# Performance work log

Measured on AMD Instinct MI355X. Metric: run time of the kernel, lower is better.

Reference implementation:

```python
import jax, jax.numpy as jnp
import numpy as np

N_NODES = 100000
N_EDGES = 1600000
IN_DIM = 64
HID_DIM = 64
OUT_DIM = 1


def setup_inputs() -> dict:
    key = jax.random.key(0)
    ks = jax.random.split(key, 5)
    x = jax.random.normal(ks[0], (N_NODES, IN_DIM), dtype=jnp.float32)
    edge_index = jax.random.randint(ks[1], (2, N_EDGES), 0, N_NODES, dtype=jnp.int64)
    s1 = 1.0 / np.sqrt(IN_DIM)
    s2 = 1.0 / np.sqrt(HID_DIM)
    W1 = jax.random.normal(ks[2], (IN_DIM, HID_DIM), dtype=jnp.float32) * s1
    b1 = jnp.zeros((HID_DIM,), dtype=jnp.float32)
    W2 = jax.random.normal(ks[3], (HID_DIM, HID_DIM), dtype=jnp.float32) * s2
    b2 = jnp.zeros((HID_DIM,), dtype=jnp.float32)
    Wp = jax.random.normal(ks[4], (HID_DIM, OUT_DIM), dtype=jnp.float32) * s2
    bp = jnp.zeros((OUT_DIM,), dtype=jnp.float32)
    return {"x": x, "edge_index": edge_index, "W1": W1, "b1": b1,
            "W2": W2, "b2": b2, "Wp": Wp, "bp": bp}


def _gcn_conv(x, src, dst, deg_inv_sqrt, W, b):
    # PyG GCNConv: linear transform, then deg-normalized scatter-add aggregation
    h = x @ W  # [N, out]
    norm = deg_inv_sqrt[src] * deg_inv_sqrt[dst]  # [E_total]
    msg = h[src] * norm[:, None]  # gather + scale, [E_total, out]
    agg = jax.ops.segment_sum(msg, dst, num_segments=x.shape[0])
    return agg + b


def reference(x, edge_index, W1, b1, W2, b2, Wp, bp):
    n = x.shape[0]
    # add self-loops (as PyG GCNConv does by default)
    loop = jnp.arange(n, dtype=edge_index.dtype)
    src = jnp.concatenate([edge_index[0], loop])
    dst = jnp.concatenate([edge_index[1], loop])
    # symmetric normalization from in-degree over dst (includes self-loops)
    deg = jax.ops.segment_sum(jnp.ones_like(dst, dtype=x.dtype), dst, num_segments=n)
    deg_inv_sqrt = jnp.where(deg > 0, jax.lax.rsqrt(jnp.maximum(deg, 1e-12)), 0.0)
    h = jax.nn.relu(_gcn_conv(x, src, dst, deg_inv_sqrt, W1, b1))
    # dropout(p=0.3) is identity at eval time
    h = jax.nn.relu(_gcn_conv(h, src, dst, deg_inv_sqrt, W2, b2))
    return h @ Wp + bp  # [N, OUT_DIM]
```

## Files before the change

kernel.cpp:

```cpp
#include <hip/hip_runtime.h>
#include <hip/hip_fp16.h>


#define GNN_N 100000
#define GNN_E 1600000
#define NBUCK 391
#define HBLK  500
#define EPBH  3200
#define NBLK  250
#define EPB   6400
#define SCTILE 16
#define STAGE_CAP 4864
#define DUMMY_OFF (GNN_N * 128)

typedef _Float16 half8 __attribute__((ext_vector_type(8)));
typedef float f32x4 __attribute__((ext_vector_type(4)));

__global__ __launch_bounds__(256) void k_hist(const int* __restrict__ dst,
                                              int* __restrict__ hist,
                                              __half* __restrict__ TA,
                                              __half* __restrict__ TB) {
    __shared__ int h[NBUCK];
    for (int i = threadIdx.x; i < NBUCK; i += 256) h[i] = 0;
    if (blockIdx.x == 0 && threadIdx.x < 16) {
        uint4 z = {0, 0, 0, 0};
        int t = threadIdx.x;
        __half* base = (t < 8) ? TA : TB;
        *(uint4*)((char*)base + DUMMY_OFF + (t & 7) * 16) = z;
    }
    __syncthreads();
    int b = blockIdx.x;
    int e0 = b * EPBH, e1 = min(e0 + EPBH, GNN_E);
    for (int e = e0 + threadIdx.x * 4; e < e1; e += 1024) {
        int4 d = *(const int4*)(dst + e);
        atomicAdd(&h[d.x >> 8], 1);
        atomicAdd(&h[d.y >> 8], 1);
        atomicAdd(&h[d.z >> 8], 1);
        atomicAdd(&h[d.w >> 8], 1);
    }
    __syncthreads();
    for (int i = threadIdx.x; i < NBUCK; i += 256)
        hist[b * NBUCK + i] = h[i];
}

__global__ __launch_bounds__(256) void k_cscan(int* __restrict__ hist,
                                               int* __restrict__ tot) {
    __shared__ int tile[256][SCTILE + 1];
    int k0 = blockIdx.x * SCTILE;
    int b = threadIdx.x;
    int lane = b & 63, w = b >> 6;
    int cSub = lane >> 4;
    int l16 = lane & 15;
    int col = w * 4 + cSub;
    int run = 0;
    for (int pass = 0; pass < 2; ++pass) {
        int r = pass * 256 + b;
#pragma unroll
        for (int i = 0; i < SCTILE; ++i) {
            int k = k0 + i;
            tile[b][i] = (k < NBUCK && r < HBLK) ? hist[r * NBUCK + k] : 0;
        }
        __syncthreads();
        for (int chunk = 0; chunk < 16; ++chunk) {
            int idx = chunk * 16 + l16;
            int v = tile[idx][col];
            int s = v;
#pragma unroll
            for (int o = 1; o < 16; o <<= 1) {
                int t = __shfl_up(s, o);
                if (l16 >= o) s += t;
            }
            tile[idx][col] = s - v + run;
            run += __shfl(s, lane | 15);
        }
        __syncthreads();
#pragma unroll
        for (int i = 0; i < SCTILE; ++i) {
            int k = k0 + i;
            if (k < NBUCK && r < HBLK) hist[r * NBUCK + k] = tile[b][i];
        }
        __syncthreads();
    }
    if (l16 == 0 && k0 + col < NBUCK) tot[k0 + col] = run;
}

__global__ __launch_bounds__(512) void k_btot(const int* __restrict__ tot,
                                              int* __restrict__ bbase,
                                              int* __restrict__ cbase) {
    __shared__ int s[512];
    int t = threadIdx.x;
    int own = (t < NBUCK) ? tot[t] : 0;
    s[t] = own;
    __syncthreads();
    for (int off = 1; off < 512; off <<= 1) {
        int v = (t >= off) ? s[t - off] : 0;
        __syncthreads();
        s[t] += v;
        __syncthreads();
    }
    if (t < NBUCK) {
        int ex = s[t] - own;
        bbase[t] = ex;
        cbase[t] = (ex & ~3) + t * 772;
    }
    if (t == 0) bbase[NBUCK] = GNN_E;
}

__global__ __launch_bounds__(256) void k_part(const int* __restrict__ src,
                                              const int* __restrict__ dst,
                                              const int* __restrict__ hist,
                                              const int* __restrict__ bbase,
                                              unsigned int* __restrict__ part) {
    __shared__ int off[NBUCK];
    int b = blockIdx.x;
    for (int i = threadIdx.x; i < NBUCK; i += 256)
        off[i] = bbase[i] + hist[(2 * b) * NBUCK + i];
    __syncthreads();
    int e0 = b * EPB, e1 = min(e0 + EPB, GNN_E);
    for (int e = e0 + threadIdx.x * 4; e < e1; e += 1024) {
        int4 d = *(const int4*)(dst + e);
        int4 s = *(const int4*)(src + e);
        int sl0 = atomicAdd(&off[d.x >> 8], 1);
        part[sl0] = ((unsigned int)(d.x & 255) << 17) | (unsigned int)s.x;
        int sl1 = atomicAdd(&off[d.y >> 8], 1);
        part[sl1] = ((unsigned int)(d.y & 255) << 17) | (unsigned int)s.y;
        int sl2 = atomicAdd(&off[d.z >> 8], 1);
        part[sl2] = ((unsigned int)(d.z & 255) << 17) | (unsigned int)s.z;
        int sl3 = atomicAdd(&off[d.w >> 8], 1);
        part[sl3] = ((unsigned int)(d.w & 255) << 17) | (unsigned int)s.w;
    }
}

__global__ __launch_bounds__(256) void k_bsort(const unsigned int* __restrict__ part,
                                               const int* __restrict__ bbase,
                                               const int* __restrict__ cbase,
                                               int* __restrict__ csr,
                                               int* __restrict__ rowptr,
                                               int* __restrict__ deg,
                                               float* __restrict__ dis) {
    __shared__ int cnt[256];
    __shared__ int pstart[256];
    __shared__ int bump[256];
    __shared__ int wtot[4];
    __shared__ unsigned int stage[STAGE_CAP];
    int k = blockIdx.x;
    int t = threadIdx.x;
    cnt[t] = 0;
    __syncthreads();
    int e0 = bbase[k], e1 = bbase[k + 1];
    int m = e1 - e0;
    bool fits = (m <= STAGE_CAP);
    for (int i = t; i < m; i += 256) {
        unsigned int p = part[e0 + i];
        if (fits) stage[i] = p;
        atomicAdd(&cnt[p >> 17], 1);
    }
    __syncthreads();
    int c = cnt[t];
    int padded = (c + 3) & ~3;
    int v = padded;
#pragma unroll
    for (int o = 1; o < 64; o <<= 1) {
        int u = __shfl_up(v, o);
        if ((t & 63) >= o) v += u;
    }
    if ((t & 63) == 63) wtot[t >> 6] = v;
    __syncthreads();
    int wb = 0;
#pragma unroll
    for (int j = 0; j < 4; ++j)
        if (j < (t >> 6)) wb += wtot[j];
    pstart[t] = wb + v - padded;
    bump[t] = pstart[t];
    __syncthreads();
    int cb = cbase[k];
    int node = k * 256 + t;
    if (node < GNN_N) {
        rowptr[node] = cb + pstart[t];
        deg[node]    = padded;
        dis[node]    = rsqrtf((float)c + 1.0f);
    }
    for (int i = t; i < m; i += 256) {
        unsigned int p = fits ? stage[i] : part[e0 + i];
        int slot = atomicAdd(&bump[p >> 17], 1);
        csr[cb + slot] = (int)(p & 0x1FFFF) << 7;
    }
    __syncthreads();
    if (node < GNN_N) {
        for (int i = c; i < padded; ++i)
            csr[cb + pstart[t] + i] = DUMMY_OFF;
    }
}

__global__ __launch_bounds__(256) void k_mmf(const float* __restrict__ X,
                                             const float* __restrict__ W,
                                             const float* __restrict__ dis,
                                             __half* __restrict__ Y, int n) {
    __shared__ __align__(16) __half Xs[64][72];
    __shared__ __align__(16) __half Wt[64][72];
    __shared__ float disS[64];
    int tid = threadIdx.x;
    int base = blockIdx.x * 64;
    for (int i = tid; i < 4096; i += 256) {
        int k = i >> 6, j = i & 63;
        Wt[j][k] = __float2half(W[i]);
    }
    if (tid < 64) disS[tid] = (base + tid < n) ? dis[base + tid] : 0.f;
#pragma unroll
    for (int ii = 0; ii < 4; ++ii) {
        int i = ii * 256 + tid;
        int r = i >> 4, c4 = i & 15;
        int row = base + r;
        float4 vv = (row < n) ? ((const float4*)(X + (size_t)row * 64))[c4]
                              : make_float4(0.f, 0.f, 0.f, 0.f);
        *(__half2*)&Xs[r][c4 * 4 + 0] = __floats2half2_rn(vv.x, vv.y);
        *(__half2*)&Xs[r][c4 * 4 + 2] = __floats2half2_rn(vv.z, vv.w);
    }
    __syncthreads();
    int w = tid >> 6, lane = tid & 63;
    int ar = w * 16 + (lane & 15);
    int ak = (lane >> 4) * 8;
    half8 a0 = *(const half8*)&Xs[ar][ak];
    half8 a1 = *(const half8*)&Xs[ar][32 + ak];
    f32x4 acc0 = {0.f, 0.f, 0.f, 0.f}, acc1 = acc0, acc2 = acc0, acc3 = acc0;
#define MMCOL(ACC, C) {                                                   \
        half8 b0 = *(const half8*)&Wt[(C) * 16 + (lane & 15)][ak];        \
        half8 b1 = *(const half8*)&Wt[(C) * 16 + (lane & 15)][32 + ak];   \
        ACC = __builtin_amdgcn_mfma_f32_16x16x32_f16(a0, b0, ACC, 0, 0, 0); \
        ACC = __builtin_amdgcn_mfma_f32_16x16x32_f16(a1, b1, ACC, 0, 0, 0); }
    MMCOL(acc0, 0) MMCOL(acc1, 1) MMCOL(acc2, 2) MMCOL(acc3, 3)
#undef MMCOL
    __syncthreads();
#define DST(ACC, C) {                                                     \
        _Pragma("unroll")                                                 \
        for (int i = 0; i < 4; ++i) {                                     \
            int rl = w * 16 + (lane >> 4) * 4 + i;                        \
            Xs[rl][(C) * 16 + (lane & 15)] = __float2half(ACC[i] * disS[rl]); \
        } }
    DST(acc0, 0) DST(acc1, 1) DST(acc2, 2) DST(acc3, 3)
#undef DST
    __syncthreads();
#pragma unroll
    for (int ii = 0; ii < 2; ++ii) {
        int i = ii * 256 + tid;
        int r = i >> 3, c8 = i & 7;
        int row = base + r;
        if (row < n)
            *(uint4*)(Y + (size_t)row * 64 + c8 * 8) = *(const uint4*)&Xs[r][c8 * 8];
    }
}

#define ACC8(A, U) {                                                     \
    float2 f_;                                                           \
    f_ = __half22float2(*(__half2*)&U.x); A[0] += f_.x; A[1] += f_.y;    \
    f_ = __half22float2(*(__half2*)&U.y); A[2] += f_.x; A[3] += f_.y;    \
    f_ = __half22float2(*(__half2*)&U.z); A[4] += f_.x; A[5] += f_.y;    \
    f_ = __half22float2(*(__half2*)&U.w); A[6] += f_.x; A[7] += f_.y; }

__global__ __launch_bounds__(256) void k_gatherW2(
        const __half* __restrict__ T, const int* __restrict__ csr,
        const int* __restrict__ rowptr, const int* __restrict__ deg,
        const float* __restrict__ dis, const float* __restrict__ bias,
        const float* __restrict__ W2, __half* __restrict__ TB) {
    __shared__ __align__(16) __half Wt[64][72];
    __shared__ __align__(16) __half Rt[32][72];
    __shared__ float disT[32];
    int tid = threadIdx.x;
    for (int i = tid; i < 4096; i += 256) {
        int k = i >> 6, j = i & 63;
        Wt[j][k] = __float2half(W2[i]);
    }
    int q = tid & 7;
    int nl = tid >> 3;
    int node = blockIdx.x * 32 + nl;
    int base = rowptr[node];
    int cnt  = deg[node];
    float dd = dis[node];
    if (q == 0) disT[nl] = dd;
    const char* Tq = (const char*)T + q * 16;
    float a0[8], a1[8];
#pragma unroll
    for (int i = 0; i < 8; ++i) { a0[i] = 0.f; a1[i] = 0.f; }
    int j = 0;
    for (; j + 8 <= cnt; j += 8) {
        int4 c0 = *(const int4*)(csr + base + j);
        int4 c1 = *(const int4*)(csr + base + j + 4);
        uint4 u0 = *(const uint4*)(Tq + (size_t)(unsigned)c0.x);
        uint4 u1 = *(const uint4*)(Tq + (size_t)(unsigned)c0.y);
        uint4 u2 = *(const uint4*)(Tq + (size_t)(unsigned)c0.z);
        uint4 u3 = *(const uint4*)(Tq + (size_t)(unsigned)c0.w);
        uint4 u4 = *(const uint4*)(Tq + (size_t)(unsigned)c1.x);
        uint4 u5 = *(const uint4*)(Tq + (size_t)(unsigned)c1.y);
        uint4 u6 = *(const uint4*)(Tq + (size_t)(unsigned)c1.z);
        uint4 u7 = *(const uint4*)(Tq + (size_t)(unsigned)c1.w);
        ACC8(a0, u0) ACC8(a1, u1) ACC8(a0, u2) ACC8(a1, u3)
        ACC8(a0, u4) ACC8(a1, u5) ACC8(a0, u6) ACC8(a1, u7)
    }
    if (j < cnt) {
        int4 c0 = *(const int4*)(csr + base + j);
        uint4 u0 = *(const uint4*)(Tq + (size_t)(unsigned)c0.x);
        uint4 u1 = *(const uint4*)(Tq + (size_t)(unsigned)c0.y);
        uint4 u2 = *(const uint4*)(Tq + (size_t)(unsigned)c0.z);
        uint4 u3 = *(const uint4*)(Tq + (size_t)(unsigned)c0.w);
        ACC8(a0, u0) ACC8(a1, u1) ACC8(a0, u2) ACC8(a1, u3)
    }
    uint4 us = *(const uint4*)(Tq + (size_t)node * 128);
    ACC8(a1, us)
    float4 bb0 = ((const float4*)bias)[q * 2 + 0];
    float4 bb1 = ((const float4*)bias)[q * 2 + 1];
    float r[8];
    r[0] = fmaxf(dd * (a0[0] + a1[0]) + bb0.x, 0.f);
    r[1] = fmaxf(dd * (a0[1] + a1[1]) + bb0.y, 0.f);
    r[2] = fmaxf(dd * (a0[2] + a1[2]) + bb0.z, 0.f);
    r[3] = fmaxf(dd * (a0[3] + a1[3]) + bb0.w, 0.f);
    r[4] = fmaxf(dd * (a0[4] + a1[4]) + bb1.x, 0.f);
    r[5] = fmaxf(dd * (a0[5] + a1[5]) + bb1.y, 0.f);
    r[6] = fmaxf(dd * (a0[6] + a1[6]) + bb1.z, 0.f);
    r[7] = fmaxf(dd * (a0[7] + a1[7]) + bb1.w, 0.f);
    uint4 u;
    *(__half2*)&u.x = __floats2half2_rn(r[0], r[1]);
    *(__half2*)&u.y = __floats2half2_rn(r[2], r[3]);
    *(__half2*)&u.z = __floats2half2_rn(r[4], r[5]);
    *(__half2*)&u.w = __floats2half2_rn(r[6], r[7]);
    *(uint4*)&Rt[nl][q * 8] = u;
    __syncthreads();
    int w = tid >> 6, lane = tid & 63;
    int band = w >> 1, cg = w & 1;
    int ar = band * 16 + (lane & 15);
    int ak = (lane >> 4) * 8;
    half8 fa0 = *(const half8*)&Rt[ar][ak];
    half8 fa1 = *(const half8*)&Rt[ar][32 + ak];
    f32x4 acc0 = {0.f, 0.f, 0.f, 0.f}, acc1 = acc0;
    {
        int c0 = cg * 2, c1 = cg * 2 + 1;
        half8 b00 = *(const half8*)&Wt[c0 * 16 + (lane & 15)][ak];
        half8 b01 = *(const half8*)&Wt[c0 * 16 + (lane & 15)][32 + ak];
        half8 b10 = *(const half8*)&Wt[c1 * 16 + (lane & 15)][ak];
        half8 b11 = *(const half8*)&Wt[c1 * 16 + (lane & 15)][32 + ak];
        acc0 = __builtin_amdgcn_mfma_f32_16x16x32_f16(fa0, b00, acc0, 0, 0, 0);
        acc0 = __builtin_amdgcn_mfma_f32_16x16x32_f16(fa1, b01, acc0, 0, 0, 0);
        acc1 = __builtin_amdgcn_mfma_f32_16x16x32_f16(fa0, b10, acc1, 0, 0, 0);
        acc1 = __builtin_amdgcn_mfma_f32_16x16x32_f16(fa1, b11, acc1, 0, 0, 0);
    }
    __syncthreads();
#pragma unroll
    for (int i = 0; i < 4; ++i) {
        int rl = band * 16 + (lane >> 4) * 4 + i;
        float dsc = disT[rl];
        Rt[rl][(cg * 2 + 0) * 16 + (lane & 15)] = __float2half(acc0[i] * dsc);
        Rt[rl][(cg * 2 + 1) * 16 + (lane & 15)] = __float2half(acc1[i] * dsc);
    }
    __syncthreads();
    {
        int r8 = tid >> 3, c8 = tid & 7;
        int row = blockIdx.x * 32 + r8;
        *(uint4*)(TB + (size_t)row * 64 + c8 * 8) = *(const uint4*)&Rt[r8][c8 * 8];
    }
}

__global__ __launch_bounds__(256) void k_gatherg(
        const __half* __restrict__ T, const int* __restrict__ csr,
        const int* __restrict__ rowptr, const int* __restrict__ deg,
        const float* __restrict__ dis, const float* __restrict__ bias,
        const float* __restrict__ Wp, const float* __restrict__ bp,
        float* __restrict__ out, int n) {
    int tid = threadIdx.x;
    int q = tid & 7;
    int node = blockIdx.x * 32 + (tid >> 3);
    if (node >= n) return;
    int base = rowptr[node];
    int cnt  = deg[node];
    float dd = dis[node];
    const char* Tq = (const char*)T + q * 16;
    float a0[8], a1[8];
#pragma unroll
    for (int i = 0; i < 8; ++i) { a0[i] = 0.f; a1[i] = 0.f; }
    int j = 0;
    for (; j + 8 <= cnt; j += 8) {
        int4 c0 = *(const int4*)(csr + base + j);
        int4 c1 = *(const int4*)(csr + base + j + 4);
        uint4 u0 = *(const uint4*)(Tq + (size_t)(unsigned)c0.x);
        uint4 u1 = *(const uint4*)(Tq + (size_t)(unsigned)c0.y);
        uint4 u2 = *(const uint4*)(Tq + (size_t)(unsigned)c0.z);
        uint4 u3 = *(const uint4*)(Tq + (size_t)(unsigned)c0.w);
        uint4 u4 = *(const uint4*)(Tq + (size_t)(unsigned)c1.x);
        uint4 u5 = *(const uint4*)(Tq + (size_t)(unsigned)c1.y);
        uint4 u6 = *(const uint4*)(Tq + (size_t)(unsigned)c1.z);
        uint4 u7 = *(const uint4*)(Tq + (size_t)(unsigned)c1.w);
        ACC8(a0, u0) ACC8(a1, u1) ACC8(a0, u2) ACC8(a1, u3)
        ACC8(a0, u4) ACC8(a1, u5) ACC8(a0, u6) ACC8(a1, u7)
    }
    if (j < cnt) {
        int4 c0 = *(const int4*)(csr + base + j);
        uint4 u0 = *(const uint4*)(Tq + (size_t)(unsigned)c0.x);
        uint4 u1 = *(const uint4*)(Tq + (size_t)(unsigned)c0.y);
        uint4 u2 = *(const uint4*)(Tq + (size_t)(unsigned)c0.z);
        uint4 u3 = *(const uint4*)(Tq + (size_t)(unsigned)c0.w);
        ACC8(a0, u0) ACC8(a1, u1) ACC8(a0, u2) ACC8(a1, u3)
    }
    uint4 us = *(const uint4*)(Tq + (size_t)node * 128);
    ACC8(a1, us)
    float4 bb0 = ((const float4*)bias)[q * 2 + 0];
    float4 bb1 = ((const float4*)bias)[q * 2 + 1];
    float r[8];
    r[0] = fmaxf(dd * (a0[0] + a1[0]) + bb0.x, 0.f);
    r[1] = fmaxf(dd * (a0[1] + a1[1]) + bb0.y, 0.f);
    r[2] = fmaxf(dd * (a0[2] + a1[2]) + bb0.z, 0.f);
    r[3] = fmaxf(dd * (a0[3] + a1[3]) + bb0.w, 0.f);
    r[4] = fmaxf(dd * (a0[4] + a1[4]) + bb1.x, 0.f);
    r[5] = fmaxf(dd * (a0[5] + a1[5]) + bb1.y, 0.f);
    r[6] = fmaxf(dd * (a0[6] + a1[6]) + bb1.z, 0.f);
    r[7] = fmaxf(dd * (a0[7] + a1[7]) + bb1.w, 0.f);
    float4 w0 = ((const float4*)Wp)[q * 2 + 0];
    float4 w1 = ((const float4*)Wp)[q * 2 + 1];
    float s = r[0] * w0.x + r[1] * w0.y + r[2] * w0.z + r[3] * w0.w
            + r[4] * w1.x + r[5] * w1.y + r[6] * w1.z + r[7] * w1.w;
#pragma unroll
    for (int m = 1; m <= 4; m <<= 1) s += __shfl_xor(s, m);
    if (q == 0) out[node] = s + bp[0];
}

extern "C" void kernel_launch(void* const* d_in, const int* in_sizes, int n_in,
                              void* d_out, int out_size, void* d_ws, size_t ws_size,
                              hipStream_t stream) {
    const float* x  = (const float*)d_in[0];
    const int*   ei = (const int*)d_in[1];
    const float* W1 = (const float*)d_in[2];
    const float* b1 = (const float*)d_in[3];
    const float* W2 = (const float*)d_in[4];
    const float* b2 = (const float*)d_in[5];
    const float* Wp = (const float*)d_in[6];
    const float* bp = (const float*)d_in[7];
    float* out = (float*)d_out;

    const int N = GNN_N, E = GNN_E;
    const int* srcv = ei;
    const int* dstv = ei + E;

    char* ws = (char*)d_ws;
    int*    hist   = (int*)(ws + 0);
    int*    bbase  = (int*)(ws + 784000);
    int*    cbase  = (int*)(ws + 785600);
    int*    rowptr = (int*)(ws + 787200);
    int*    deg    = (int*)(ws + 1187200);
    float*  dis    = (float*)(ws + 1587200);
    int*    tot    = (int*)(ws + 1587200);
    int*    csr    = (int*)(ws + 1987200);
    __half* TA     = (__half*)(ws + 9597440);
    __half* TB     = (__half*)(ws + 22400000);
    unsigned int* part = (unsigned int*)(ws + 35200256);

    k_hist <<<HBLK, 256, 0, stream>>>(dstv, hist, TA, TB);
    k_cscan<<<(NBUCK + SCTILE - 1) / SCTILE, 256, 0, stream>>>(hist, tot);
    k_btot <<<1, 512, 0, stream>>>(tot, bbase, cbase);
    k_part <<<NBLK, 256, 0, stream>>>(srcv, dstv, hist, bbase, part);
    k_bsort<<<NBUCK, 256, 0, stream>>>(part, bbase, cbase, csr, rowptr, deg, dis);

    k_mmf<<<(N + 63) / 64, 256, 0, stream>>>(x, W1, dis, TA, N);
    k_gatherW2<<<N / 32, 256, 0, stream>>>(TA, csr, rowptr, deg, dis, b1, W2, TB);
    k_gatherg<<<(N + 31) / 32, 256, 0, stream>>>(TB, csr, rowptr, deg, dis,
                                                 b2, Wp, bp, out, N);
}
```

Baseline: 127.5 us.

## Fuse CSR build kernels into one cooperative kernel with grid syncs

Merges the five CSR construction kernels (histogram, column scan, bucket total scan, partition, bucket sort) into a single cooperative launch separated by grid-wide barriers, with shared memory overlaid through a union. This removes four kernel launch boundaries and their gaps. The partition phase now uses 500 blocks of 3200 edges instead of 250 blocks of 6400, matching the histogram granularity. The trade-off is grid.sync cost, a larger LDS footprint (about 21 KB for the staging buffer) held by every block, and a requirement that all 500 blocks be co-resident.

Result: slower. 361.6 us (+183.5%).

```diff
diff --git a/kernel.cpp b/kernel.cpp
--- a/kernel.cpp
+++ b/kernel.cpp
@@ -1,14 +1,15 @@
 #include <hip/hip_runtime.h>
 #include <hip/hip_fp16.h>
+#include <hip/hip_cooperative_groups.h>
+
+namespace cg = cooperative_groups;
 
 
 #define GNN_N 100000
 #define GNN_E 1600000
 #define NBUCK 391
-#define HBLK  500
-#define EPBH  3200
-#define NBLK  250
-#define EPB   6400
+#define CBLK  500
+#define EPB   3200
 #define SCTILE 16
 #define STAGE_CAP 4864
 #define DUMMY_OFF (GNN_N * 128)
@@ -16,179 +17,195 @@
 typedef _Float16 half8 __attribute__((ext_vector_type(8)));
 typedef float f32x4 __attribute__((ext_vector_type(4)));
 
-__global__ __launch_bounds__(256) void k_hist(const int* __restrict__ dst,
-                                              int* __restrict__ hist,
-                                              __half* __restrict__ TA,
-                                              __half* __restrict__ TB) {
-    __shared__ int h[NBUCK];
-    for (int i = threadIdx.x; i < NBUCK; i += 256) h[i] = 0;
-    if (blockIdx.x == 0 && threadIdx.x < 16) {
+union CsrLds {
+    int h[NBUCK];
+    int tile[256][SCTILE + 1];
+    int s[512];
+    int off[NBUCK];
+    struct {
+        int cnt[256];
+        int pstart[256];
+        int bump[256];
+        int wtot[4];
+        unsigned int stage[STAGE_CAP];
+    } p5;
+};
+
+__global__ __launch_bounds__(256) void k_csr(const int* __restrict__ src,
+                                             const int* __restrict__ dst,
+                                             int* __restrict__ hist,
+                                             int* __restrict__ bbase,
+                                             int* __restrict__ cbase,
+                                             int* __restrict__ tot,
+                                             unsigned int* __restrict__ part,
+                                             int* __restrict__ csr,
+                                             int* __restrict__ rowptr,
+                                             int* __restrict__ deg,
+                                             float* __restrict__ dis,
+                                             __half* __restrict__ TA,
+                                             __half* __restrict__ TB) {
+    cg::grid_group grid = cg::this_grid();
+    __shared__ CsrLds u;
+    int bid = blockIdx.x;
+    int t = threadIdx.x;
+
+    for (int i = t; i < NBUCK; i += 256) u.h[i] = 0;
+    if (bid == 0 && t < 16) {
         uint4 z = {0, 0, 0, 0};
-        int t = threadIdx.x;
         __half* base = (t < 8) ? TA : TB;
         *(uint4*)((char*)base + DUMMY_OFF + (t & 7) * 16) = z;
     }
     __syncthreads();
-    int b = blockIdx.x;
-    int e0 = b * EPBH, e1 = min(e0 + EPBH, GNN_E);
-    for (int e = e0 + threadIdx.x * 4; e < e1; e += 1024) {
-        int4 d = *(const int4*)(dst + e);
-        atomicAdd(&h[d.x >> 8], 1);
-        atomicAdd(&h[d.y >> 8], 1);
-        atomicAdd(&h[d.z >> 8], 1);
-        atomicAdd(&h[d.w >> 8], 1);
-    }
-    __syncthreads();
-    for (int i = threadIdx.x; i < NBUCK; i += 256)
-        hist[b * NBUCK + i] = h[i];
-}
-
-__global__ __launch_bounds__(256) void k_cscan(int* __restrict__ hist,
-                                               int* __restrict__ tot) {
-    __shared__ int tile[256][SCTILE + 1];
-    int k0 = blockIdx.x * SCTILE;
-    int b = threadIdx.x;
-    int lane = b & 63, w = b >> 6;
-    int cSub = lane >> 4;
-    int l16 = lane & 15;
-    int col = w * 4 + cSub;
-    int run = 0;
-    for (int pass = 0; pass < 2; ++pass) {
-        int r = pass * 256 + b;
-#pragma unroll
-        for (int i = 0; i < SCTILE; ++i) {
-            int k = k0 + i;
-            tile[b][i] = (k < NBUCK && r < HBLK) ? hist[r * NBUCK + k] : 0;
-        }
-        __syncthreads();
-        for (int chunk = 0; chunk < 16; ++chunk) {
-            int idx = chunk * 16 + l16;
-            int v = tile[idx][col];
-            int s = v;
-#pragma unroll
-            for (int o = 1; o < 16; o <<= 1) {
-                int t = __shfl_up(s, o);
-                if (l16 >= o) s += t;
+    {
+        int e0 = bid * EPB, e1 = min(e0 + EPB, GNN_E);
+        for (int e = e0 + t * 4; e < e1; e += 1024) {
+            int4 d = *(const int4*)(dst + e);
+            atomicAdd(&u.h[d.x >> 8], 1);
+            atomicAdd(&u.h[d.y >> 8], 1);
+            atomicAdd(&u.h[d.z >> 8], 1);
+            atomicAdd(&u.h[d.w >> 8], 1);
+        }
+        __syncthreads();
+        for (int i = t; i < NBUCK; i += 256)
+            hist[bid * NBUCK + i] = u.h[i];
+    }
+    grid.sync();
+
+    if (bid < (NBUCK + SCTILE - 1) / SCTILE) {
+        int k0 = bid * SCTILE;
+        int lane = t & 63, w = t >> 6;
+        int cSub = lane >> 4;
+        int l16 = lane & 15;
+        int col = w * 4 + cSub;
+        int run = 0;
+        for (int pass = 0; pass < 2; ++pass) {
+            int r = pass * 256 + t;
+#pragma unroll
+            for (int i = 0; i < SCTILE; ++i) {
+                int k = k0 + i;
+                u.tile[t][i] = (k < NBUCK && r < CBLK) ? hist[r * NBUCK + k] : 0;
             }
-            tile[idx][col] = s - v + run;
-            run += __shfl(s, lane | 15);
-        }
-        __syncthreads();
-#pragma unroll
-        for (int i = 0; i < SCTILE; ++i) {
-            int k = k0 + i;
-            if (k < NBUCK && r < HBLK) hist[r * NBUCK + k] = tile[b][i];
-        }
-        __syncthreads();
-    }
-    if (l16 == 0 && k0 + col < NBUCK) tot[k0 + col] = run;
-}
-
-__global__ __launch_bounds__(512) void k_btot(const int* __restrict__ tot,
-                                              int* __restrict__ bbase,
-                                              int* __restrict__ cbase) {
-    __shared__ int s[512];
-    int t = threadIdx.x;
-    int own = (t < NBUCK) ? tot[t] : 0;
-    s[t] = own;
-    __syncthreads();
-    for (int off = 1; off < 512; off <<= 1) {
-        int v = (t >= off) ? s[t - off] : 0;
-        __syncthreads();
-        s[t] += v;
-        __syncthreads();
-    }
-    if (t < NBUCK) {
-        int ex = s[t] - own;
-        bbase[t] = ex;
-        cbase[t] = (ex & ~3) + t * 772;
-    }
-    if (t == 0) bbase[NBUCK] = GNN_E;
-}
-
-__global__ __launch_bounds__(256) void k_part(const int* __restrict__ src,
-                                              const int* __restrict__ dst,
-                                              const int* __restrict__ hist,
-                                              const int* __restrict__ bbase,
-                                              unsigned int* __restrict__ part) {
-    __shared__ int off[NBUCK];
-    int b = blockIdx.x;
-    for (int i = threadIdx.x; i < NBUCK; i += 256)
-        off[i] = bbase[i] + hist[(2 * b) * NBUCK + i];
-    __syncthreads();
-    int e0 = b * EPB, e1 = min(e0 + EPB, GNN_E);
-    for (int e = e0 + threadIdx.x * 4; e < e1; e += 1024) {
-        int4 d = *(const int4*)(dst + e);
-        int4 s = *(const int4*)(src + e);
-        int sl0 = atomicAdd(&off[d.x >> 8], 1);
-        part[sl0] = ((unsigned int)(d.x & 255) << 17) | (unsigned int)s.x;
-        int sl1 = atomicAdd(&off[d.y >> 8], 1);
-        part[sl1] = ((unsigned int)(d.y & 255) << 17) | (unsigned int)s.y;
-        int sl2 = atomicAdd(&off[d.z >> 8], 1);
-        part[sl2] = ((unsigned int)(d.z & 255) << 17) | (unsigned int)s.z;
-        int sl3 = atomicAdd(&off[d.w >> 8], 1);
-        part[sl3] = ((unsigned int)(d.w & 255) << 17) | (unsigned int)s.w;
-    }
-}
-
-__global__ __launch_bounds__(256) void k_bsort(const unsigned int* __restrict__ part,
-                                               const int* __restrict__ bbase,
-                                               const int* __restrict__ cbase,
-                                               int* __restrict__ csr,
-                                               int* __restrict__ rowptr,
-                                               int* __restrict__ deg,
-                                               float* __restrict__ dis) {
-    __shared__ int cnt[256];
-    __shared__ int pstart[256];
-    __shared__ int bump[256];
-    __shared__ int wtot[4];
-    __shared__ unsigned int stage[STAGE_CAP];
-    int k = blockIdx.x;
-    int t = threadIdx.x;
-    cnt[t] = 0;
-    __syncthreads();
-    int e0 = bbase[k], e1 = bbase[k + 1];
-    int m = e1 - e0;
-    bool fits = (m <= STAGE_CAP);
-    for (int i = t; i < m; i += 256) {
-        unsigned int p = part[e0 + i];
-        if (fits) stage[i] = p;
-        atomicAdd(&cnt[p >> 17], 1);
-    }
-    __syncthreads();
-    int c = cnt[t];
-    int padded = (c + 3) & ~3;
-    int v = padded;
-#pragma unroll
-    for (int o = 1; o < 64; o <<= 1) {
-        int u = __shfl_up(v, o);
-        if ((t & 63) >= o) v += u;
-    }
-    if ((t & 63) == 63) wtot[t >> 6] = v;
-    __syncthreads();
-    int wb = 0;
-#pragma unroll
-    for (int j = 0; j < 4; ++j)
-        if (j < (t >> 6)) wb += wtot[j];
-    pstart[t] = wb + v - padded;
-    bump[t] = pstart[t];
-    __syncthreads();
-    int cb = cbase[k];
-    int node = k * 256 + t;
-    if (node < GNN_N) {
-        rowptr[node] = cb + pstart[t];
-        deg[node]    = padded;
-        dis[node]    = rsqrtf((float)c + 1.0f);
-    }
-    for (int i = t; i < m; i += 256) {
-        unsigned int p = fits ? stage[i] : part[e0 + i];
-        int slot = atomicAdd(&bump[p >> 17], 1);
-        csr[cb + slot] = (int)(p & 0x1FFFF) << 7;
-    }
-    __syncthreads();
-    if (node < GNN_N) {
-        for (int i = c; i < padded; ++i)
-            csr[cb + pstart[t] + i] = DUMMY_OFF;
+            __syncthreads();
+            for (int chunk = 0; chunk < 16; ++chunk) {
+                int idx = chunk * 16 + l16;
+                int v = u.tile[idx][col];
+                int s = v;
+#pragma unroll
+                for (int o = 1; o < 16; o <<= 1) {
+                    int tt = __shfl_up(s, o);
+                    if (l16 >= o) s += tt;
+                }
+                u.tile[idx][col] = s - v + run;
+                run += __shfl(s, lane | 15);
+            }
+            __syncthreads();
+#pragma unroll
+            for (int i = 0; i < SCTILE; ++i) {
+                int k = k0 + i;
+                if (k < NBUCK && r < CBLK) hist[r * NBUCK + k] = u.tile[t][i];
+            }
+            __syncthreads();
+        }
+        if (l16 == 0 && k0 + col < NBUCK) tot[k0 + col] = run;
+    }
+    grid.sync();
+
+    if (bid == 0) {
+        int own0 = (t < NBUCK) ? tot[t] : 0;
+        int own1 = (t + 256 < NBUCK) ? tot[t + 256] : 0;
+        u.s[t] = own0;
+        u.s[t + 256] = own1;
+        __syncthreads();
+        for (int off = 1; off < 512; off <<= 1) {
+            int a = (t >= off) ? u.s[t - off] : 0;
+            int b = (t + 256 >= off) ? u.s[t + 256 - off] : 0;
+            __syncthreads();
+            u.s[t] += a;
+            u.s[t + 256] += b;
+            __syncthreads();
+        }
+        if (t < NBUCK) {
+            int ex = u.s[t] - own0;
+            bbase[t] = ex;
+            cbase[t] = (ex & ~3) + t * 772;
+        }
+        if (t + 256 < NBUCK) {
+            int ex = u.s[t + 256] - own1;
+            bbase[t + 256] = ex;
+            cbase[t + 256] = (ex & ~3) + (t + 256) * 772;
+        }
+        if (t == 0) bbase[NBUCK] = GNN_E;
+    }
+    grid.sync();
+
+    for (int i = t; i < NBUCK; i += 256)
+        u.off[i] = bbase[i] + hist[bid * NBUCK + i];
+    __syncthreads();
+    {
+        int e0 = bid * EPB, e1 = min(e0 + EPB, GNN_E);
+        for (int e = e0 + t * 4; e < e1; e += 1024) {
+            int4 d = *(const int4*)(dst + e);
+            int4 s = *(const int4*)(src + e);
+            int sl0 = atomicAdd(&u.off[d.x >> 8], 1);
+            part[sl0] = ((unsigned int)(d.x & 255) << 17) | (unsigned int)s.x;
+            int sl1 = atomicAdd(&u.off[d.y >> 8], 1);
+            part[sl1] = ((unsigned int)(d.y & 255) << 17) | (unsigned int)s.y;
+            int sl2 = atomicAdd(&u.off[d.z >> 8], 1);
+            part[sl2] = ((unsigned int)(d.z & 255) << 17) | (unsigned int)s.z;
+            int sl3 = atomicAdd(&u.off[d.w >> 8], 1);
+            part[sl3] = ((unsigned int)(d.w & 255) << 17) | (unsigned int)s.w;
+        }
+    }
+    grid.sync();
+
+    if (bid < NBUCK) {
+        int k = bid;
+        u.p5.cnt[t] = 0;
+        __syncthreads();
+        int e0 = bbase[k], e1 = bbase[k + 1];
+        int m = e1 - e0;
+        bool fits = (m <= STAGE_CAP);
+        for (int i = t; i < m; i += 256) {
+            unsigned int p = part[e0 + i];
+            if (fits) u.p5.stage[i] = p;
+            atomicAdd(&u.p5.cnt[p >> 17], 1);
+        }
+        __syncthreads();
+        int c = u.p5.cnt[t];
+        int padded = (c + 3) & ~3;
+        int v = padded;
+#pragma unroll
+        for (int o = 1; o < 64; o <<= 1) {
+            int uu = __shfl_up(v, o);
+            if ((t & 63) >= o) v += uu;
+        }
+        if ((t & 63) == 63) u.p5.wtot[t >> 6] = v;
+        __syncthreads();
+        int wb = 0;
+#pragma unroll
+        for (int j = 0; j < 4; ++j)
+            if (j < (t >> 6)) wb += u.p5.wtot[j];
+        int ps = wb + v - padded;
+        u.p5.pstart[t] = ps;
+        u.p5.bump[t] = ps;
+        __syncthreads();
+        int cb = cbase[k];
+        int node = k * 256 + t;
+        if (node < GNN_N) {
+            rowptr[node] = cb + ps;
+            deg[node]    = padded;
+            dis[node]    = rsqrtf((float)c + 1.0f);
+        }
+        for (int i = t; i < m; i += 256) {
+            unsigned int p = fits ? u.p5.stage[i] : part[e0 + i];
+            int slot = atomicAdd(&u.p5.bump[p >> 17], 1);
+            csr[cb + slot] = (int)(p & 0x1FFFF) << 7;
+        }
+        __syncthreads();
+        if (node < GNN_N) {
+            for (int i = c; i < padded; ++i)
+                csr[cb + ps + i] = DUMMY_OFF;
+        }
     }
 }
 
@@ -325,14 +342,14 @@
     *(uint4*)&Rt[nl][q * 8] = u;
     __syncthreads();
     int w = tid >> 6, lane = tid & 63;
-    int band = w >> 1, cg = w & 1;
+    int band = w >> 1, cg2 = w & 1;
     int ar = band * 16 + (lane & 15);
     int ak = (lane >> 4) * 8;
     half8 fa0 = *(const half8*)&Rt[ar][ak];
     half8 fa1 = *(const half8*)&Rt[ar][32 + ak];
     f32x4 acc0 = {0.f, 0.f, 0.f, 0.f}, acc1 = acc0;
     {
-        int c0 = cg * 2, c1 = cg * 2 + 1;
+        int c0 = cg2 * 2, c1 = cg2 * 2 + 1;
         half8 b00 = *(const half8*)&Wt[c0 * 16 + (lane & 15)][ak];
         half8 b01 = *(const half8*)&Wt[c0 * 16 + (lane & 15)][32 + ak];
         half8 b10 = *(const half8*)&Wt[c1 * 16 + (lane & 15)][ak];
@@ -347,8 +364,8 @@
     for (int i = 0; i < 4; ++i) {
         int rl = band * 16 + (lane >> 4) * 4 + i;
         float dsc = disT[rl];
-        Rt[rl][(cg * 2 + 0) * 16 + (lane & 15)] = __float2half(acc0[i] * dsc);
-        Rt[rl][(cg * 2 + 1) * 16 + (lane & 15)] = __float2half(acc1[i] * dsc);
+        Rt[rl][(cg2 * 2 + 0) * 16 + (lane & 15)] = __float2half(acc0[i] * dsc);
+        Rt[rl][(cg2 * 2 + 1) * 16 + (lane & 15)] = __float2half(acc1[i] * dsc);
     }
     __syncthreads();
     {
@@ -450,11 +467,14 @@
     __half* TB     = (__half*)(ws + 22400000);
     unsigned int* part = (unsigned int*)(ws + 35200256);
 
-    k_hist <<<HBLK, 256, 0, stream>>>(dstv, hist, TA, TB);
-    k_cscan<<<(NBUCK + SCTILE - 1) / SCTILE, 256, 0, stream>>>(hist, tot);
-    k_btot <<<1, 512, 0, stream>>>(tot, bbase, cbase);
-    k_part <<<NBLK, 256, 0, stream>>>(srcv, dstv, hist, bbase, part);
-    k_bsort<<<NBUCK, 256, 0, stream>>>(part, bbase, cbase, csr, rowptr, deg, dis);
+    {
+        void* args[] = {(void*)&srcv, (void*)&dstv, (void*)&hist, (void*)&bbase,
+                        (void*)&cbase, (void*)&tot, (void*)&part, (void*)&csr,
+                        (void*)&rowptr, (void*)&deg, (void*)&dis, (void*)&TA,
+                        (void*)&TB};
+        hipLaunchCooperativeKernel((void*)k_csr, dim3(CBLK), dim3(256),
+                                   args, 0, stream);
+    }
 
     k_mmf<<<(N + 63) / 64, 256, 0, stream>>>(x, W1, dis, TA, N);
     k_gatherW2<<<N / 32, 256, 0, stream>>>(TA, csr, rowptr, deg, dis, b1, W2, TB);
```
